# Optimization experiments

Hardware: AMD Instinct MI355X
Metric: run time of the kernel (lower is better)

Reference implementation:

```python
import jax, jax.numpy as jnp
import numpy as np

N, E, D, R = 50000, 800000, 64, 65


def setup_inputs() -> dict:
    key = jax.random.key(0)
    ks = jax.random.split(key, 8)
    x = jax.random.normal(ks[0], (N, D), dtype=jnp.float32)
    src = jax.random.randint(ks[1], (E,), 0, N, dtype=jnp.int32)
    dst = jax.random.randint(ks[2], (E,), 0, N, dtype=jnp.int32)
    edge_type = jax.random.randint(ks[3], (E,), 0, R, dtype=jnp.int32)
    s = 1.0 / np.sqrt(D)
    W1 = jax.random.normal(ks[4], (R, D, D), dtype=jnp.float32) * s
    Wl1 = jax.random.normal(ks[5], (D, D), dtype=jnp.float32) * s
    W2 = jax.random.normal(ks[6], (R, D, D), dtype=jnp.float32) * s
    Wl2 = jax.random.normal(ks[7], (D, D), dtype=jnp.float32) * s
    return {"x": x, "src": src, "dst": dst, "edge_type": edge_type,
            "W1": W1, "Wl1": Wl1, "W2": W2, "Wl2": Wl2}


def _rgcn_layer(x, src, dst, edge_type, W, Wl):
    # x: [N, D_in], W: [R, D_in, D_out], Wl: [D_in, D_out]
    n = x.shape[0]
    r = W.shape[0]
    # per-relation transform of all node features: [R, N, D_out]
    xw = jnp.einsum('nd,rdh->rnh', x, W)
    # gather transformed source feature for each edge by its relation: [E, D_out]
    msg = xw[edge_type, src]
    # mean aggregation per (destination node, relation) as in PyG RGCNConv
    key = dst.astype(jnp.int32) * r + edge_type
    cnt = jax.ops.segment_sum(jnp.ones(key.shape, x.dtype), key, num_segments=n * r)
    norm = 1.0 / jnp.maximum(cnt[key], 1.0)  # [E]
    agg = jax.ops.segment_sum(msg * norm[:, None], dst, num_segments=n)  # [N, D_out]
    # self-loop linear term (self_loop_weights in original module)
    out = agg + x @ Wl
    # activation; dropout is identity in eval mode; batch norm disabled
    return jax.nn.relu(out)


def reference(x, src, dst, edge_type, W1, Wl1, W2, Wl2):
    h = _rgcn_layer(x, src, dst, edge_type, W1, Wl1)
    h = _rgcn_layer(h, src, dst, edge_type, W2, Wl2)
    return h
```

## Files before the change

### kernel.cpp

```cpp
#include <hip/hip_runtime.h>

typedef __attribute__((ext_vector_type(8))) short bf16x8;
typedef __attribute__((ext_vector_type(4))) float f32x4;
typedef __attribute__((ext_vector_type(2))) unsigned int u32x2;

constexpr int D = 64;
constexpr int SEG = 64;
constexpr int CSTR = 16;

__device__ inline unsigned short f2bf(float f) {
  unsigned u = __float_as_uint(f);
  u += 0x7fff + ((u >> 16) & 1);
  return (unsigned short)(u >> 16);
}
__device__ inline float bflo(unsigned u) { return __uint_as_float(u << 16); }
__device__ inline float bfhi(unsigned u) { return __uint_as_float(u & 0xffff0000u); }

__global__ __launch_bounds__(256) void count_kernel(
    const int* __restrict__ dst, const int* __restrict__ et,
    int* __restrict__ bcnt, int* __restrict__ deg, int E, int R, int nbE) {
  __shared__ int lh[128];
  int t = threadIdx.x;
  if (t < 128) lh[t] = 0;
  __syncthreads();
  int e = blockIdx.x * 256 + t;
  if (e < E) {
    atomicAdd(&deg[(long)dst[e] * CSTR], 1);
    atomicAdd(&lh[et[e]], 1);
  }
  __syncthreads();
  if (t < R) bcnt[t * nbE + blockIdx.x] = lh[t];
}

__global__ __launch_bounds__(256) void scanA_dual_kernel(
    const int* __restrict__ bcnt, const int* __restrict__ deg,
    int* __restrict__ bsum, int nBC, int N, int nbBC) {
  __shared__ int s[256];
  int t = threadIdx.x;
  int b = blockIdx.x;
  int v;
  if (b < nbBC) {
    int i = b * 256 + t;
    v = (i < nBC) ? bcnt[i] : 0;
  } else {
    int i = (b - nbBC) * 256 + t;
    v = (i < N) ? deg[(long)i * CSTR] : 0;
  }
  s[t] = v;
  __syncthreads();
  for (int o = 128; o > 0; o >>= 1) {
    if (t < o) s[t] += s[t + o];
    __syncthreads();
  }
  if (t == 0) bsum[b] = s[0];
}

__device__ inline void scanB_region(int* bsum, int nb, int t) {
  __shared__ int s[256];
  __shared__ int carry;
  if (t == 0) carry = 0;
  __syncthreads();
  for (int base = 0; base < nb; base += 256) {
    int i = base + t;
    int v = (i < nb) ? bsum[i] : 0;
    s[t] = v;
    __syncthreads();
    for (int o = 1; o < 256; o <<= 1) {
      int u = (t >= o) ? s[t - o] : 0;
      __syncthreads();
      s[t] += u;
      __syncthreads();
    }
    if (i < nb) bsum[i] = carry + s[t] - v;
    __syncthreads();
    if (t == 0) carry += s[255];
    __syncthreads();
  }
}

__global__ __launch_bounds__(256) void scanB_dual_kernel(
    int* __restrict__ bsum, int nbBC, int nbN) {
  int t = threadIdx.x;
  scanB_region(bsum, nbBC, t);
  scanB_region(bsum + nbBC, nbN, t);
}

__global__ __launch_bounds__(256) void scanC_dual_kernel(
    const int* __restrict__ bcnt, const int* __restrict__ deg,
    const int* __restrict__ bsum, int* __restrict__ prefE,
    int* __restrict__ dstoff, int* __restrict__ cur2,
    int nBC, int N, int nbBC) {
  __shared__ int s[256];
  int t = threadIdx.x;
  int b = blockIdx.x;
  bool isBC = (b < nbBC);
  int i = (isBC ? b : b - nbBC) * 256 + t;
  int n = isBC ? nBC : N;
  int v = 0;
  if (i < n) v = isBC ? bcnt[i] : deg[(long)i * CSTR];
  s[t] = v;
  __syncthreads();
  for (int o = 1; o < 256; o <<= 1) {
    int u = (t >= o) ? s[t - o] : 0;
    __syncthreads();
    s[t] += u;
    __syncthreads();
  }
  int excl = bsum[b] + s[t] - v;
  if (isBC) {
    if (i < n) prefE[i] = excl;
    if (i == n - 1) prefE[n] = excl + v;
  } else {
    if (i < n) { dstoff[i] = excl; cur2[(long)i * CSTR] = excl; }
    if (i == n - 1) dstoff[n] = excl + v;
  }
}

__global__ void prefix_wrel_kernel(const int* __restrict__ prefE,
                                   int* __restrict__ cursor, int* __restrict__ wrel,
                                   int2* __restrict__ eidx,
                                   int nbE, int R, int Ecap, int nwavesTot) {
  __shared__ int sc[128];
  int l = threadIdx.x;
  int tot = 0, c = 0;
  if (l < R) {
    tot = prefE[(l + 1) * nbE] - prefE[l * nbE];
    c = (tot + SEG - 1) & ~(SEG - 1);
  }
  sc[l] = c;
  __syncthreads();
  for (int ofs = 1; ofs < 128; ofs <<= 1) {
    int v = (l >= ofs) ? sc[l - ofs] : 0;
    __syncthreads();
    sc[l] += v;
    __syncthreads();
  }
  if (l < R) {
    int cur = sc[l] - c;
    cursor[l] = cur;
    int w0 = cur >> 6;
    int nw = c >> 6;
    for (int w = 0; w < nw; ++w) wrel[w0 + w] = l;
    for (int p = cur + tot; p < cur + c; ++p) eidx[p] = make_int2(-1, -1);
  }
  int total = sc[127];
  for (int p = total + l; p < Ecap; p += 128) eidx[p] = make_int2(-1, -1);
  for (int w = (total >> 6) + l; w < nwavesTot; w += 128) wrel[w] = 0;
}

__global__ __launch_bounds__(256) void scatter_kernel(
    const int* __restrict__ src, const int* __restrict__ dst, const int* __restrict__ et,
    const int* __restrict__ cursor, const int* __restrict__ prefE,
    int* __restrict__ cur2, int2* __restrict__ eidx, int* __restrict__ relrow,
    int E, int R, int nbE) {
  __shared__ int lh[128];
  __shared__ int lbase[128];
  int t = threadIdx.x, b = blockIdx.x;
  if (t < R) {
    lh[t] = 0;
    lbase[t] = cursor[t] + prefE[t * nbE + b] - prefE[t * nbE];
  }
  __syncthreads();
  int e = b * 256 + t;
  if (e < E) {
    int r = et[e], s = src[e], d = dst[e];
    int lr = atomicAdd(&lh[r], 1);
    int jd = atomicAdd(&cur2[(long)d * CSTR], 1);
    int pos = lbase[r] + lr;
    eidx[pos] = make_int2(s, jd);
    relrow[jd] = r;
  }
}

__global__ __launch_bounds__(256) void cvt_all_kernel(
    const float* __restrict__ x, unsigned short* __restrict__ xb, int nx,
    const float* __restrict__ W1, unsigned short* __restrict__ WT1,
    const float* __restrict__ W2, unsigned short* __restrict__ WT2, int nw,
    const float* __restrict__ Wl1, unsigned short* __restrict__ WTl1,
    const float* __restrict__ Wl2, unsigned short* __restrict__ WTl2, int nl) {
  int i = blockIdx.x * 256 + threadIdx.x;
  if (i < nx) { xb[i] = f2bf(x[i]); return; }
  i -= nx;
  if (i < 2 * nw) {
    const float* W = (i < nw) ? W1 : W2;
    unsigned short* WT = (i < nw) ? WT1 : WT2;
    int i2 = (i < nw) ? i : i - nw;
    int n = i2 & 63, k = (i2 >> 6) & 63, r = i2 >> 12;
    WT[(r << 12) + (n << 6) + k] = f2bf(W[(r << 12) + (k << 6) + n]);
    return;
  }
  i -= 2 * nw;
  if (i < 2 * nl) {
    const float* W = (i < nl) ? Wl1 : Wl2;
    unsigned short* WT = (i < nl) ? WTl1 : WTl2;
    int i2 = (i < nl) ? i : i - nl;
    int n = i2 & 63, k = (i2 >> 6) & 63;
    WT[(n << 6) + k] = f2bf(W[(k << 6) + n]);
  }
}

__global__ __launch_bounds__(256)
void msg_kernel(const unsigned short* __restrict__ xb,
                const unsigned short* __restrict__ WT,
                const int2* __restrict__ eidx, const int* __restrict__ wrel,
                unsigned int* __restrict__ msgp, int nwaves) {
  const int lane = (int)threadIdx.x & 63;
  const int l15 = lane & 15;
  const int q = lane >> 4;
  const int nwg = (int)gridDim.x;
  const int bid = (int)blockIdx.x;
  const int xcd = bid & 7, idx = bid >> 3;
  const int qq = nwg >> 3, rr = nwg & 7;
  const int swz = (xcd < rr ? xcd * (qq + 1) : rr * (qq + 1) + (xcd - rr) * qq) + idx;
  const int wave = swz * 4 + ((int)threadIdx.x >> 6);
  if (wave >= nwaves) return;
  const long base = (long)wave * SEG;
  const int r = wrel[wave];
  const unsigned short* wb = WT + ((long)r << 12);
  bf16x8 Bf[4][2];
#pragma unroll
  for (int nt = 0; nt < 4; ++nt)
#pragma unroll
    for (int kh = 0; kh < 2; ++kh)
      Bf[nt][kh] = *(const bf16x8*)(wb + (nt * 16 + l15) * 64 + kh * 32 + q * 8);
#pragma unroll
  for (int t = 0; t < 4; ++t) {
    int2 rec = eidx[base + t * 16 + l15];
    const unsigned short* xr = xb + ((long)max(rec.x, 0) << 6);
    bf16x8 A0 = *(const bf16x8*)(xr + q * 8);
    bf16x8 A1 = *(const bf16x8*)(xr + 32 + q * 8);
    f32x4 acc0 = (f32x4)0.0f, acc1 = (f32x4)0.0f, acc2 = (f32x4)0.0f, acc3 = (f32x4)0.0f;
    acc0 = __builtin_amdgcn_mfma_f32_16x16x32_bf16(A0, Bf[0][0], acc0, 0, 0, 0);
    acc0 = __builtin_amdgcn_mfma_f32_16x16x32_bf16(A1, Bf[0][1], acc0, 0, 0, 0);
    acc1 = __builtin_amdgcn_mfma_f32_16x16x32_bf16(A0, Bf[1][0], acc1, 0, 0, 0);
    acc1 = __builtin_amdgcn_mfma_f32_16x16x32_bf16(A1, Bf[1][1], acc1, 0, 0, 0);
    acc2 = __builtin_amdgcn_mfma_f32_16x16x32_bf16(A0, Bf[2][0], acc2, 0, 0, 0);
    acc2 = __builtin_amdgcn_mfma_f32_16x16x32_bf16(A1, Bf[2][1], acc2, 0, 0, 0);
    acc3 = __builtin_amdgcn_mfma_f32_16x16x32_bf16(A0, Bf[3][0], acc3, 0, 0, 0);
    acc3 = __builtin_amdgcn_mfma_f32_16x16x32_bf16(A1, Bf[3][1], acc3, 0, 0, 0);
#pragma unroll
    for (int rg = 0; rg < 4; ++rg) {
      int row = q * 4 + rg;
      int jd = __shfl(rec.y, row);
      if (jd >= 0) {
        unsigned p0 = (unsigned)f2bf(acc0[rg]) | ((unsigned)f2bf(acc1[rg]) << 16);
        unsigned p1 = (unsigned)f2bf(acc2[rg]) | ((unsigned)f2bf(acc3[rg]) << 16);
        u32x2 pk;
        pk.x = p0; pk.y = p1;
        *(u32x2*)(msgp + (long)jd * 32 + 2 * l15) = pk;
      }
    }
  }
}

__global__ __launch_bounds__(256) void weight_kernel(
    const int* __restrict__ relrow, const int* __restrict__ dstoff,
    float* __restrict__ wrow, int N) {
  __shared__ int rsh[4][256];
  const int wv = (int)threadIdx.x >> 6;
  const int lane = (int)threadIdx.x & 63;
  const int d = blockIdx.x * 4 + wv;
  if (d >= N) return;
  const int off = dstoff[d], end = dstoff[d + 1];
  const int deg = end - off;
  if (deg <= 0) return;
  if (deg <= 256) {
    const int nit = (deg + 63) >> 6;
    for (int it = 0; it < nit; ++it) {
      int l = it * 64 + lane;
      if (l < deg) rsh[wv][l] = relrow[off + l];
    }
    __threadfence_block();
    for (int it = 0; it < nit; ++it) {
      int l = it * 64 + lane;
      if (l < deg) {
        int rv = rsh[wv][l];
        int c = 0;
        for (int m = 0; m < deg; ++m) c += (rsh[wv][m] == rv) ? 1 : 0;
        wrow[off + l] = 1.0f / (float)c;
      }
    }
  } else {
    for (int l = lane; l < deg; l += 64) {
      int rv = relrow[off + l];
      int c = 0;
      for (int m = off; m < end; ++m) c += (relrow[m] == rv) ? 1 : 0;
      wrow[off + l] = 1.0f / (float)c;
    }
  }
}

__global__ __launch_bounds__(256) void aggsl_kernel(
    const unsigned int* __restrict__ msgp, const int* __restrict__ dstoff,
    const float* __restrict__ wrow,
    const unsigned short* __restrict__ xbin, const unsigned short* __restrict__ WTl,
    float* __restrict__ outp, unsigned short* __restrict__ hb, int N) {
  __shared__ float aggs[64][66];
  const int lane = (int)threadIdx.x & 63;
  const int wv = (int)threadIdx.x >> 6;
  const int base = blockIdx.x * 64;
  const int j = lane & 31;
  const int half = lane >> 5;
  for (int i16 = 0; i16 < 16; ++i16) {
    const int d = base + wv * 16 + i16;
    if (d >= N) break;
    const int off = dstoff[d], end = dstoff[d + 1];
    float a0 = 0.f, a1 = 0.f, b0 = 0.f, b1 = 0.f;
    float c0 = 0.f, c1 = 0.f, e0 = 0.f, e1 = 0.f;
    int i = off + half;
    for (; i + 6 < end; i += 8) {
      float w0 = wrow[i];
      float w1 = wrow[i + 2];
      float w2 = wrow[i + 4];
      float w3 = wrow[i + 6];
      unsigned u0 = msgp[(long)i * 32 + j];
      unsigned u1 = msgp[(long)(i + 2) * 32 + j];
      unsigned u2 = msgp[(long)(i + 4) * 32 + j];
      unsigned u3 = msgp[(long)(i + 6) * 32 + j];
      a0 = fmaf(w0, bflo(u0), a0);
      a1 = fmaf(w0, bfhi(u0), a1);
      b0 = fmaf(w1, bflo(u1), b0);
      b1 = fmaf(w1, bfhi(u1), b1);
      c0 = fmaf(w2, bflo(u2), c0);
      c1 = fmaf(w2, bfhi(u2), c1);
      e0 = fmaf(w3, bflo(u3), e0);
      e1 = fmaf(w3, bfhi(u3), e1);
    }
    for (; i + 2 < end; i += 4) {
      float w0 = wrow[i];
      float w1 = wrow[i + 2];
      unsigned u0 = msgp[(long)i * 32 + j];
      unsigned u1 = msgp[(long)(i + 2) * 32 + j];
      a0 = fmaf(w0, bflo(u0), a0);
      a1 = fmaf(w0, bfhi(u0), a1);
      b0 = fmaf(w1, bflo(u1), b0);
      b1 = fmaf(w1, bfhi(u1), b1);
    }
    if (i < end) {
      float w0 = wrow[i];
      unsigned u0 = msgp[(long)i * 32 + j];
      a0 = fmaf(w0, bflo(u0), a0);
      a1 = fmaf(w0, bfhi(u0), a1);
    }
    float aLo = (a0 + b0) + (c0 + e0), aHi = (a1 + b1) + (c1 + e1);
    aLo += __shfl_xor(aLo, 32);
    aHi += __shfl_xor(aHi, 32);
    if (half == 0) {
      const int k = j >> 1;
      const int colLo = (j & 1) ? 32 + k : k;
      aggs[d - base][colLo] = aLo;
      aggs[d - base][colLo + 16] = aHi;
    }
  }
  __syncthreads();
  const int l15 = lane & 15;
  const int q = lane >> 4;
  const int row0 = base + wv * 16;
  if (row0 >= N) return;
  bf16x8 Bf[4][2];
#pragma unroll
  for (int nt = 0; nt < 4; ++nt)
#pragma unroll
    for (int kh = 0; kh < 2; ++kh)
      Bf[nt][kh] = *(const bf16x8*)(WTl + (nt * 16 + l15) * 64 + kh * 32 + q * 8);
  const int m = min(row0 + l15, N - 1);
  const unsigned short* xr = xbin + ((long)m << 6);
  bf16x8 A0 = *(const bf16x8*)(xr + q * 8);
  bf16x8 A1 = *(const bf16x8*)(xr + 32 + q * 8);
  f32x4 acc[4];
#pragma unroll
  for (int nt = 0; nt < 4; ++nt)
#pragma unroll
    for (int rg = 0; rg < 4; ++rg) {
      int node = row0 + q * 4 + rg;
      acc[nt][rg] = (node < N) ? aggs[wv * 16 + q * 4 + rg][nt * 16 + l15] : 0.0f;
    }
#pragma unroll
  for (int nt = 0; nt < 4; ++nt) {
    acc[nt] = __builtin_amdgcn_mfma_f32_16x16x32_bf16(A0, Bf[nt][0], acc[nt], 0, 0, 0);
    acc[nt] = __builtin_amdgcn_mfma_f32_16x16x32_bf16(A1, Bf[nt][1], acc[nt], 0, 0, 0);
  }
#pragma unroll
  for (int rg = 0; rg < 4; ++rg) {
    int node = row0 + q * 4 + rg;
    if (node < N) {
#pragma unroll
      for (int nt = 0; nt < 4; ++nt) {
        float v = fmaxf(acc[nt][rg], 0.0f);
        if (outp) outp[(long)node * D + nt * 16 + l15] = v;
        if (hb) hb[(long)node * D + nt * 16 + l15] = f2bf(v);
      }
    }
  }
}

extern "C" void kernel_launch(void* const* d_in, const int* in_sizes, int n_in,
                              void* d_out, int out_size, void* d_ws, size_t ws_size,
                              hipStream_t stream) {
  const float* x   = (const float*)d_in[0];
  const int* src   = (const int*)d_in[1];
  const int* dst   = (const int*)d_in[2];
  const int* et    = (const int*)d_in[3];
  const float* W1  = (const float*)d_in[4];
  const float* Wl1 = (const float*)d_in[5];
  const float* W2  = (const float*)d_in[6];
  const float* Wl2 = (const float*)d_in[7];
  float* out = (float*)d_out;

  const int N = in_sizes[0] / D;
  const int E = in_sizes[1];
  const int R = in_sizes[4] / (D * D);

  const int Ecap = ((E + SEG - 1) & ~(SEG - 1)) + R * SEG;
  const int nwaves = Ecap / SEG;
  const int nbN = (N + 255) / 256;
  const int nbE = (E + 255) / 256;
  const int nBC = R * nbE;
  const int nbBC = (nBC + 255) / 256;

  char* ws = (char*)d_ws;
  size_t off = 0;
  auto alloc = [&](size_t bytes) -> void* {
    void* p = (void*)(ws + off);
    off += (bytes + 255) & ~(size_t)255;
    return p;
  };
  int*   cursor = (int*)alloc((size_t)R * sizeof(int));
  int*   deg    = (int*)alloc((size_t)N * CSTR * sizeof(int));
  int*   cur2   = (int*)alloc((size_t)N * CSTR * sizeof(int));
  int*   bcnt   = (int*)alloc((size_t)nBC * sizeof(int));
  int*   prefE  = (int*)alloc((size_t)(nBC + 1) * sizeof(int));
  int*   bsum   = (int*)alloc((size_t)(nbBC + nbN) * sizeof(int));
  int*   dstoff = (int*)alloc((size_t)(N + 1) * sizeof(int));
  int*   relrow = (int*)alloc((size_t)E * sizeof(int));
  float* wrow   = (float*)alloc((size_t)E * sizeof(float));
  int*   wrel   = (int*)alloc((size_t)nwaves * sizeof(int));
  int2*  eidx   = (int2*)alloc((size_t)(Ecap + SEG) * sizeof(int2));
  unsigned int* msgp = (unsigned int*)alloc((size_t)E * 32 * sizeof(unsigned int));
  unsigned short* xb  = (unsigned short*)alloc((size_t)N * D * sizeof(unsigned short));
  unsigned short* hb  = (unsigned short*)alloc((size_t)N * D * sizeof(unsigned short));
  unsigned short* WT1 = (unsigned short*)alloc((size_t)R * D * D * sizeof(unsigned short));
  unsigned short* WT2 = (unsigned short*)alloc((size_t)R * D * D * sizeof(unsigned short));
  unsigned short* WTl1 = (unsigned short*)alloc((size_t)D * D * sizeof(unsigned short));
  unsigned short* WTl2 = (unsigned short*)alloc((size_t)D * D * sizeof(unsigned short));
  (void)ws_size; (void)n_in; (void)out_size;

  const int msg_blocks = (nwaves + 3) / 4;
  const int w_blocks = (N + 3) / 4;
  const int aggsl_blocks = (N + 63) / 64;
  const int nx = N * D;
  const int nw = R * D * D;
  const int nl = D * D;
  const int cvt_total = nx + 2 * nw + 2 * nl;

  hipMemsetAsync(deg, 0, (size_t)N * CSTR * sizeof(int), stream);
  count_kernel<<<nbE, 256, 0, stream>>>(dst, et, bcnt, deg, E, R, nbE);
  scanA_dual_kernel<<<nbBC + nbN, 256, 0, stream>>>(bcnt, deg, bsum, nBC, N, nbBC);
  scanB_dual_kernel<<<1, 256, 0, stream>>>(bsum, nbBC, nbN);
  scanC_dual_kernel<<<nbBC + nbN, 256, 0, stream>>>(bcnt, deg, bsum, prefE,
                                                    dstoff, cur2, nBC, N, nbBC);
  prefix_wrel_kernel<<<1, 128, 0, stream>>>(prefE, cursor, wrel, eidx,
                                            nbE, R, Ecap, nwaves);
  scatter_kernel<<<nbE, 256, 0, stream>>>(src, dst, et, cursor, prefE, cur2,
                                          eidx, relrow, E, R, nbE);
  weight_kernel<<<w_blocks, 256, 0, stream>>>(relrow, dstoff, wrow, N);
  cvt_all_kernel<<<(cvt_total + 255) / 256, 256, 0, stream>>>(
      x, xb, nx, W1, WT1, W2, WT2, nw, Wl1, WTl1, Wl2, WTl2, nl);

  msg_kernel<<<msg_blocks, 256, 0, stream>>>(xb, WT1, eidx, wrel, msgp, nwaves);
  aggsl_kernel<<<aggsl_blocks, 256, 0, stream>>>(msgp, dstoff, wrow, xb, WTl1,
                                                 nullptr, hb, N);

  msg_kernel<<<msg_blocks, 256, 0, stream>>>(hb, WT2, eidx, wrel, msgp, nwaves);
  aggsl_kernel<<<aggsl_blocks, 256, 0, stream>>>(msgp, dstoff, wrow, hb, WTl2,
                                                 out, nullptr, N);
}
```

Baseline: 343.1 us.

## Fuse conversion into scatter, move relrow write into first msg kernel, prefetch gathers

The bf16 conversion kernel is merged into the scatter kernel as extra blocks, which removes one launch and lets the two run concurrently. The relrow scatter write moves out of the scatter kernel into the first msg_kernel call, where lanes holding valid edge records write it. The msg kernel now loads all four edge records and all A-fragment gathers before the MFMA loop, giving more memory-level parallelism at the cost of extra registers. weight_kernel is reordered to run after the first msg kernel, since it depends on relrow.

Result: faster. 334.2 us (-2.6%).

```diff
diff --git a/kernel.cpp b/kernel.cpp
--- a/kernel.cpp
+++ b/kernel.cpp
@@ -148,14 +148,42 @@
   for (int w = (total >> 6) + l; w < nwavesTot; w += 128) wrel[w] = 0;
 }
 
-__global__ __launch_bounds__(256) void scatter_kernel(
+__global__ __launch_bounds__(256) void scatter_cvt_kernel(
     const int* __restrict__ src, const int* __restrict__ dst, const int* __restrict__ et,
     const int* __restrict__ cursor, const int* __restrict__ prefE,
-    int* __restrict__ cur2, int2* __restrict__ eidx, int* __restrict__ relrow,
-    int E, int R, int nbE) {
+    int* __restrict__ cur2, int2* __restrict__ eidx,
+    int E, int R, int nbE,
+    const float* __restrict__ x, unsigned short* __restrict__ xb, int nx,
+    const float* __restrict__ W1, unsigned short* __restrict__ WT1,
+    const float* __restrict__ W2, unsigned short* __restrict__ WT2, int nw,
+    const float* __restrict__ Wl1, unsigned short* __restrict__ WTl1,
+    const float* __restrict__ Wl2, unsigned short* __restrict__ WTl2, int nl) {
+  int b = blockIdx.x;
+  if (b >= nbE) {
+    int i = (b - nbE) * 256 + (int)threadIdx.x;
+    if (i < nx) { xb[i] = f2bf(x[i]); return; }
+    i -= nx;
+    if (i < 2 * nw) {
+      const float* W = (i < nw) ? W1 : W2;
+      unsigned short* WT = (i < nw) ? WT1 : WT2;
+      int i2 = (i < nw) ? i : i - nw;
+      int n = i2 & 63, k = (i2 >> 6) & 63, r = i2 >> 12;
+      WT[(r << 12) + (n << 6) + k] = f2bf(W[(r << 12) + (k << 6) + n]);
+      return;
+    }
+    i -= 2 * nw;
+    if (i < 2 * nl) {
+      const float* W = (i < nl) ? Wl1 : Wl2;
+      unsigned short* WT = (i < nl) ? WTl1 : WTl2;
+      int i2 = (i < nl) ? i : i - nl;
+      int n = i2 & 63, k = (i2 >> 6) & 63;
+      WT[(n << 6) + k] = f2bf(W[(k << 6) + n]);
+    }
+    return;
+  }
   __shared__ int lh[128];
   __shared__ int lbase[128];
-  int t = threadIdx.x, b = blockIdx.x;
+  int t = threadIdx.x;
   if (t < R) {
     lh[t] = 0;
     lbase[t] = cursor[t] + prefE[t * nbE + b] - prefE[t * nbE];
@@ -168,34 +196,6 @@
     int jd = atomicAdd(&cur2[(long)d * CSTR], 1);
     int pos = lbase[r] + lr;
     eidx[pos] = make_int2(s, jd);
-    relrow[jd] = r;
-  }
-}
-
-__global__ __launch_bounds__(256) void cvt_all_kernel(
-    const float* __restrict__ x, unsigned short* __restrict__ xb, int nx,
-    const float* __restrict__ W1, unsigned short* __restrict__ WT1,
-    const float* __restrict__ W2, unsigned short* __restrict__ WT2, int nw,
-    const float* __restrict__ Wl1, unsigned short* __restrict__ WTl1,
-    const float* __restrict__ Wl2, unsigned short* __restrict__ WTl2, int nl) {
-  int i = blockIdx.x * 256 + threadIdx.x;
-  if (i < nx) { xb[i] = f2bf(x[i]); return; }
-  i -= nx;
-  if (i < 2 * nw) {
-    const float* W = (i < nw) ? W1 : W2;
-    unsigned short* WT = (i < nw) ? WT1 : WT2;
-    int i2 = (i < nw) ? i : i - nw;
-    int n = i2 & 63, k = (i2 >> 6) & 63, r = i2 >> 12;
-    WT[(r << 12) + (n << 6) + k] = f2bf(W[(r << 12) + (k << 6) + n]);
-    return;
-  }
-  i -= 2 * nw;
-  if (i < 2 * nl) {
-    const float* W = (i < nl) ? Wl1 : Wl2;
-    unsigned short* WT = (i < nl) ? WTl1 : WTl2;
-    int i2 = (i < nl) ? i : i - nl;
-    int n = i2 & 63, k = (i2 >> 6) & 63;
-    WT[(n << 6) + k] = f2bf(W[(k << 6) + n]);
   }
 }
 
@@ -203,7 +203,7 @@
 void msg_kernel(const unsigned short* __restrict__ xb,
                 const unsigned short* __restrict__ WT,
                 const int2* __restrict__ eidx, const int* __restrict__ wrel,
-                unsigned int* __restrict__ msgp, int nwaves) {
+                unsigned int* __restrict__ msgp, int* __restrict__ relrow, int nwaves) {
   const int lane = (int)threadIdx.x & 63;
   const int l15 = lane & 15;
   const int q = lane >> 4;
@@ -217,31 +217,42 @@
   const long base = (long)wave * SEG;
   const int r = wrel[wave];
   const unsigned short* wb = WT + ((long)r << 12);
+  int2 rec[4];
+#pragma unroll
+  for (int t = 0; t < 4; ++t) rec[t] = eidx[base + t * 16 + l15];
   bf16x8 Bf[4][2];
 #pragma unroll
   for (int nt = 0; nt < 4; ++nt)
 #pragma unroll
     for (int kh = 0; kh < 2; ++kh)
       Bf[nt][kh] = *(const bf16x8*)(wb + (nt * 16 + l15) * 64 + kh * 32 + q * 8);
+  bf16x8 A[4][2];
 #pragma unroll
   for (int t = 0; t < 4; ++t) {
-    int2 rec = eidx[base + t * 16 + l15];
-    const unsigned short* xr = xb + ((long)max(rec.x, 0) << 6);
-    bf16x8 A0 = *(const bf16x8*)(xr + q * 8);
-    bf16x8 A1 = *(const bf16x8*)(xr + 32 + q * 8);
+    const unsigned short* xr = xb + ((long)max(rec[t].x, 0) << 6);
+    A[t][0] = *(const bf16x8*)(xr + q * 8);
+    A[t][1] = *(const bf16x8*)(xr + 32 + q * 8);
+  }
+  if (relrow) {
+#pragma unroll
+    for (int t = 0; t < 4; ++t)
+      if (lane < 16 && rec[t].y >= 0) relrow[rec[t].y] = r;
+  }
+#pragma unroll
+  for (int t = 0; t < 4; ++t) {
     f32x4 acc0 = (f32x4)0.0f, acc1 = (f32x4)0.0f, acc2 = (f32x4)0.0f, acc3 = (f32x4)0.0f;
-    acc0 = __builtin_amdgcn_mfma_f32_16x16x32_bf16(A0, Bf[0][0], acc0, 0, 0, 0);
-    acc0 = __builtin_amdgcn_mfma_f32_16x16x32_bf16(A1, Bf[0][1], acc0, 0, 0, 0);
-    acc1 = __builtin_amdgcn_mfma_f32_16x16x32_bf16(A0, Bf[1][0], acc1, 0, 0, 0);
-    acc1 = __builtin_amdgcn_mfma_f32_16x16x32_bf16(A1, Bf[1][1], acc1, 0, 0, 0);
-    acc2 = __builtin_amdgcn_mfma_f32_16x16x32_bf16(A0, Bf[2][0], acc2, 0, 0, 0);
-    acc2 = __builtin_amdgcn_mfma_f32_16x16x32_bf16(A1, Bf[2][1], acc2, 0, 0, 0);
-    acc3 = __builtin_amdgcn_mfma_f32_16x16x32_bf16(A0, Bf[3][0], acc3, 0, 0, 0);
-    acc3 = __builtin_amdgcn_mfma_f32_16x16x32_bf16(A1, Bf[3][1], acc3, 0, 0, 0);
+    acc0 = __builtin_amdgcn_mfma_f32_16x16x32_bf16(A[t][0], Bf[0][0], acc0, 0, 0, 0);
+    acc0 = __builtin_amdgcn_mfma_f32_16x16x32_bf16(A[t][1], Bf[0][1], acc0, 0, 0, 0);
+    acc1 = __builtin_amdgcn_mfma_f32_16x16x32_bf16(A[t][0], Bf[1][0], acc1, 0, 0, 0);
+    acc1 = __builtin_amdgcn_mfma_f32_16x16x32_bf16(A[t][1], Bf[1][1], acc1, 0, 0, 0);
+    acc2 = __builtin_amdgcn_mfma_f32_16x16x32_bf16(A[t][0], Bf[2][0], acc2, 0, 0, 0);
+    acc2 = __builtin_amdgcn_mfma_f32_16x16x32_bf16(A[t][1], Bf[2][1], acc2, 0, 0, 0);
+    acc3 = __builtin_amdgcn_mfma_f32_16x16x32_bf16(A[t][0], Bf[3][0], acc3, 0, 0, 0);
+    acc3 = __builtin_amdgcn_mfma_f32_16x16x32_bf16(A[t][1], Bf[3][1], acc3, 0, 0, 0);
 #pragma unroll
     for (int rg = 0; rg < 4; ++rg) {
       int row = q * 4 + rg;
-      int jd = __shfl(rec.y, row);
+      int jd = __shfl(rec[t].y, row);
       if (jd >= 0) {
         unsigned p0 = (unsigned)f2bf(acc0[rg]) | ((unsigned)f2bf(acc1[rg]) << 16);
         unsigned p1 = (unsigned)f2bf(acc2[rg]) | ((unsigned)f2bf(acc3[rg]) << 16);
@@ -452,6 +463,7 @@
   const int nw = R * D * D;
   const int nl = D * D;
   const int cvt_total = nx + 2 * nw + 2 * nl;
+  const int cvt_blocks = (cvt_total + 255) / 256;
 
   hipMemsetAsync(deg, 0, (size_t)N * CSTR * sizeof(int), stream);
   count_kernel<<<nbE, 256, 0, stream>>>(dst, et, bcnt, deg, E, R, nbE);
@@ -461,17 +473,16 @@
                                                     dstoff, cur2, nBC, N, nbBC);
   prefix_wrel_kernel<<<1, 128, 0, stream>>>(prefE, cursor, wrel, eidx,
                                             nbE, R, Ecap, nwaves);
-  scatter_kernel<<<nbE, 256, 0, stream>>>(src, dst, et, cursor, prefE, cur2,
-                                          eidx, relrow, E, R, nbE);
+  scatter_cvt_kernel<<<nbE + cvt_blocks, 256, 0, stream>>>(
+      src, dst, et, cursor, prefE, cur2, eidx, E, R, nbE,
+      x, xb, nx, W1, WT1, W2, WT2, nw, Wl1, WTl1, Wl2, WTl2, nl);
+
+  msg_kernel<<<msg_blocks, 256, 0, stream>>>(xb, WT1, eidx, wrel, msgp, relrow, nwaves);
   weight_kernel<<<w_blocks, 256, 0, stream>>>(relrow, dstoff, wrow, N);
-  cvt_all_kernel<<<(cvt_total + 255) / 256, 256, 0, stream>>>(
-      x, xb, nx, W1, WT1, W2, WT2, nw, Wl1, WTl1, Wl2, WTl2, nl);
-
-  msg_kernel<<<msg_blocks, 256, 0, stream>>>(xb, WT1, eidx, wrel, msgp, nwaves);
   aggsl_kernel<<<aggsl_blocks, 256, 0, stream>>>(msgp, dstoff, wrow, xb, WTl1,
                                                  nullptr, hb, N);
 
-  msg_kernel<<<msg_blocks, 256, 0, stream>>>(hb, WT2, eidx, wrel, msgp, nwaves);
+  msg_kernel<<<msg_blocks, 256, 0, stream>>>(hb, WT2, eidx, wrel, msgp, nullptr, nwaves);
   aggsl_kernel<<<aggsl_blocks, 256, 0, stream>>>(msgp, dstoff, wrow, hb, WTl2,
                                                  out, nullptr, N);
 }
```
